# Optimization experiments

Hardware: AMD Instinct MI355X
Metric: run time of the kernel (lower is better)

## Reference

```python
import jax, jax.numpy as jnp
import numpy as np

# Static config (matches init_kwargs)
D_MODEL, H, L, P = 256, 8, 4, 4
HEAD_DIM = D_MODEL // H
SPATIAL = ((76, 114), (38, 57), (19, 29), (10, 15))  # (h, w) per level
NV = sum(h * w for h, w in SPATIAL)  # 11531
B, NQ = 2, NV


def setup_inputs() -> dict:
    key = jax.random.key(0)
    ks = jax.random.split(key, 12)
    inp = {
        "query": jax.random.normal(ks[0], (B, NQ, D_MODEL), jnp.float32),
        "reference_points": jax.random.uniform(ks[1], (B, NQ, L, 2), jnp.float32),
        "value": jax.random.normal(ks[2], (B, NV, D_MODEL), jnp.float32),
        # Linear params stored as [in, out] (i.e. torch weight transposed)
        "W_off": jax.random.normal(ks[3], (D_MODEL, H * L * P * 2), jnp.float32) * 0.02,
        "b_off": jax.random.normal(ks[4], (H * L * P * 2,), jnp.float32) * 0.5,
        "W_attn": jax.random.normal(ks[5], (D_MODEL, H * L * P), jnp.float32) * 0.02,
        "b_attn": jnp.zeros((H * L * P,), jnp.float32),
        "W_val": jax.random.normal(ks[6], (D_MODEL, D_MODEL), jnp.float32) * 0.05,
        "b_val": jnp.zeros((D_MODEL,), jnp.float32),
        "W_out": jax.random.normal(ks[7], (D_MODEL, D_MODEL), jnp.float32) * 0.05,
        "b_out": jnp.zeros((D_MODEL,), jnp.float32),
    }
    return inp


def _msda(query, reference_points, value, W_off, b_off, W_attn, b_attn,
          W_val, b_val, W_out, b_out):
    Bq, Nq, C = query.shape
    D = HEAD_DIM
    # value projection -> [B, H, Nv, D]
    v = (value @ W_val + b_val).reshape(Bq, -1, H, D).transpose(0, 2, 1, 3)
    # sampling locations: ref + offset / (w, h)  -> [B, Nq, H, L, P, 2] in [0,1] coords
    off = (query @ W_off + b_off).reshape(Bq, Nq, H, L, P, 2)
    wh = jnp.array([[w, h] for h, w in SPATIAL], dtype=query.dtype)  # [L, 2]
    loc = reference_points[:, :, None, :, None, :] + off / wh[None, None, None, :, None, :]
    # attention weights softmax over L*P  -> [B, H, Nq, L, P]
    attn = jax.nn.softmax((query @ W_attn + b_attn).reshape(Bq, Nq, H, L * P), axis=-1)
    attn = attn.reshape(Bq, Nq, H, L, P).transpose(0, 2, 1, 3, 4)
    starts = np.concatenate([[0], np.cumsum([h * w for h, w in SPATIAL])]).astype(int)
    out = jnp.zeros((Bq, H, Nq, D), query.dtype)
    for l, (lh, lw) in enumerate(SPATIAL):
        feat = v[:, :, starts[l]:starts[l + 1], :]  # [B, H, lh*lw, D]
        # grid_sample align_corners=False: pixel = loc * size - 0.5
        px = loc[:, :, :, l, :, 0].transpose(0, 2, 1, 3) * lw - 0.5  # [B, H, Nq, P]
        py = loc[:, :, :, l, :, 1].transpose(0, 2, 1, 3) * lh - 0.5
        x0 = jnp.floor(px)
        y0 = jnp.floor(py)
        samp = jnp.zeros(px.shape + (D,), query.dtype)
        for dx in (0, 1):
            for dy in (0, 1):
                xi = x0 + dx
                yi = y0 + dy
                w = (1.0 - jnp.abs(px - xi)) * (1.0 - jnp.abs(py - yi))
                valid = (xi >= 0) & (xi <= lw - 1) & (yi >= 0) & (yi <= lh - 1)
                idx = (jnp.clip(yi, 0, lh - 1) * lw + jnp.clip(xi, 0, lw - 1)).astype(jnp.int32)
                g = jnp.take_along_axis(feat, idx.reshape(Bq, H, -1)[..., None], axis=2)
                g = g.reshape(Bq, H, Nq, P, D)
                samp = samp + g * jnp.where(valid, w, 0.0)[..., None]
        out = out + jnp.einsum('bhnpd,bhnp->bhnd', samp, attn[:, :, :, l, :])
    out = out.transpose(0, 2, 1, 3).reshape(Bq, Nq, C)
    return out @ W_out + b_out


def reference(query, reference_points, value, W_off, b_off, W_attn, b_attn,
              W_val, b_val, W_out, b_out):
    return _msda(query, reference_points, value, W_off, b_off, W_attn, b_attn,
                 W_val, b_val, W_out, b_out)
```

## Files before the change

kernel.cpp:

```cpp
#include <hip/hip_runtime.h>
#include <cmath>

#define B_    2
#define NQ_   11531
#define NV_   11531
#define M_    (B_ * NQ_)
#define NCB_  2883

typedef unsigned short u16;
typedef unsigned int   u32;
typedef __attribute__((ext_vector_type(8))) short bf16x8;
typedef __attribute__((ext_vector_type(4))) float f32x4;
typedef __attribute__((ext_vector_type(2))) float f32x2;

__device__ __forceinline__ u16 f2bf(float f) {
    union { float f; unsigned u; } v; v.f = f;
    unsigned r = v.u + 0x7FFFu + ((v.u >> 16) & 1u);
    return (u16)(r >> 16);
}
__device__ __forceinline__ u16 f2h(float f) {
    union { _Float16 h; u16 u; } v; v.h = (_Float16)f; return v.u;
}
__device__ __forceinline__ float h2f(u16 u) {
    union { u16 u; _Float16 h; } v; v.u = u; return (float)v.h;
}
__device__ __forceinline__ f32x2 unpk(u32 u) {
    union { unsigned u; float f; } lo, hi;
    lo.u = u << 16; hi.u = u & 0xFFFF0000u;
    f32x2 r; r.x = lo.f; r.y = hi.f; return r;
}

__device__ __forceinline__ int sort_key(const float* __restrict__ refp, int bq) {
    const int b = bq / NQ_;
    const float2 r = *(const float2*)&refp[(size_t)bq * 8];
    int qx = (int)(r.x * 32.f); qx = min(max(qx, 0), 31);
    int qy = (int)(r.y * 32.f); qy = min(max(qy, 0), 31);
    return b * 1024 + qy * 32 + qx;
}

__global__ __launch_bounds__(256) void transpose_hist_cast(
    const float* __restrict__ Wv, const float* __restrict__ Wo,
    const float* __restrict__ Wa, const float* __restrict__ Wu,
    const float* __restrict__ refp,
    const float* __restrict__ query, const float* __restrict__ value,
    u16* __restrict__ Tv, u16* __restrict__ Toa, u16* __restrict__ Tu,
    int* __restrict__ hist, u16* __restrict__ qbf, u16* __restrict__ vbf) {
    const int bid = blockIdx.x;
    const int tid = threadIdx.x;
    if (bid >= 347) {
        const int t8 = bid - 347;
        const bool isq = t8 < NCB_;
        const int cb = isq ? t8 : t8 - NCB_;
        const float* S = isq ? query : value;
        u16* D = isq ? qbf : vbf;
        const size_t TOT = (size_t)M_ * 256;
        const size_t e = ((size_t)cb * 256 + tid) * 8;
        if (e + 8 <= TOT) {
            const float4 a = *(const float4*)&S[e];
            const float4 b = *(const float4*)&S[e + 4];
            ushort4 lo, hi;
            lo.x = f2bf(a.x); lo.y = f2bf(a.y); lo.z = f2bf(a.z); lo.w = f2bf(a.w);
            hi.x = f2bf(b.x); hi.y = f2bf(b.y); hi.z = f2bf(b.z); hi.w = f2bf(b.w);
            *(ushort4*)&D[e] = lo;
            *(ushort4*)&D[e + 4] = hi;
        } else {
            for (size_t i = e; i < TOT; ++i) D[i] = f2bf(S[i]);
        }
        return;
    }
    if (bid >= 256) {
        const int bq = (bid - 256) * 256 + tid;
        if (bq < M_) atomicAdd(&hist[sort_key(refp, bq)], 1);
        return;
    }
    const int z = bid >> 6;
    const float* W; u16* T; int N; int rowoff = 0;
    if (z == 0)      { W = Wv; T = Tv;  N = 256; }
    else if (z == 1) { W = Wo; T = Toa; N = 256; }
    else if (z == 2) { W = Wa; T = Toa; N = 128; rowoff = 256; }
    else             { W = Wu; T = Tu;  N = 256; }
    const int rest = bid & 63;
    const int n0 = (rest & 7) * 32, k0 = (rest >> 3) * 32;
    if (n0 >= N) return;
    __shared__ float t[32][33];
    const int c = tid & 31, r0 = tid >> 5;
#pragma unroll
    for (int i = 0; i < 4; ++i)
        t[r0 + i * 8][c] = W[(size_t)(k0 + r0 + i * 8) * N + n0 + c];
    __syncthreads();
#pragma unroll
    for (int i = 0; i < 4; ++i)
        T[(size_t)(rowoff + n0 + r0 + i * 8) * 256 + k0 + c] = f2bf(t[c][r0 + i * 8]);
}

__device__ void scan_block(const int* __restrict__ hist, int* __restrict__ ofs,
                           int* part) {
    const int tid = threadIdx.x;
    const int base = tid * 8;
    int loc[8]; int s = 0;
#pragma unroll
    for (int i = 0; i < 8; ++i) { loc[i] = s; s += hist[base + i]; }
    part[tid] = s;
    __syncthreads();
    for (int d = 1; d < 256; d <<= 1) {
        const int v = part[tid];
        const int u = (tid >= d) ? part[tid - d] : 0;
        __syncthreads();
        part[tid] = v + u;
        __syncthreads();
    }
    const int off = (tid > 0) ? part[tid - 1] : 0;
#pragma unroll
    for (int i = 0; i < 8; ++i) ofs[base + i] = off + loc[i];
}

__global__ __launch_bounds__(256) void repack_scatter(
    const u16* __restrict__ ws_v, const float* __restrict__ refp,
    int* __restrict__ ofs, int* __restrict__ perm,
    u32* __restrict__ v3, int nsc) {
    const int bid = blockIdx.x;
    const int tid = threadIdx.x;
    if (bid < nsc) {
        const int bq = bid * 256 + tid;
        if (bq < M_) {
            const int pos = atomicAdd(&ofs[sort_key(refp, bq)], 1);
            perm[pos] = bq;
        }
        return;
    }
    const int g4 = (bid - nsc) * 256 + tid;
    if (g4 >= 8 * M_ * 8) return;
    const int h = g4 / (M_ * 8);
    const int rem = g4 - h * (M_ * 8);
    const int r = rem >> 3;
    const int c = (rem & 7) * 4;
    const ushort4 lo = *(const ushort4*)&ws_v[(size_t)r * 256 + h * 32 + c];
    ushort4 hi = make_ushort4(0, 0, 0, 0);
    if (r + 1 < M_) hi = *(const ushort4*)&ws_v[(size_t)(r + 1) * 256 + h * 32 + c];
    uint4 o;
    o.x = (u32)lo.x | ((u32)hi.x << 16);
    o.y = (u32)lo.y | ((u32)hi.y << 16);
    o.z = (u32)lo.z | ((u32)hi.z << 16);
    o.w = (u32)lo.w | ((u32)hi.w << 16);
    *(uint4*)&v3[((size_t)h * M_ + r) * 32 + c] = o;
}

template <int TN, int EPI>
__device__ __forceinline__ void gemm_body(const u16* __restrict__ A,
                                          const u16* __restrict__ WT,
                                          const float* __restrict__ bias,
                                          const float* __restrict__ bias2,
                                          void* __restrict__ Cv, int M,
                                          int bm, int bn,
                                          short* A_l, short* B_l) {
    constexpr int K = 256;
    const int tid = threadIdx.x;
    const int w = tid >> 6;
    const int lane = tid & 63;
    const int wr = (w >> 1) * 64;
    const int wc = (w & 1) * 64;
    const int lr = lane & 15;

    f32x4 acc[4][4] = {};

    for (int k0 = 0; k0 < K; k0 += 64) {
#pragma unroll
        for (int i = 0; i < 4; ++i) {
            const int vid = tid + i * 256;
            const int ar = vid >> 3;
            const int ak = (vid & 7) * 8;
            const int gr = bm + ar;
            uint4 hv = make_uint4(0u, 0u, 0u, 0u);
            if (gr < M) hv = *(const uint4*)&A[(size_t)gr * K + k0 + ak];
            *(uint4*)&A_l[ar * 72 + ak] = hv;
        }
#pragma unroll
        for (int i = 0; i < 4; ++i) {
            const int vid = tid + i * 256;
            const int nr = vid >> 3;
            const int kk = (vid & 7) * 8;
            const uint4 wv = *(const uint4*)&WT[(size_t)(bn + nr) * K + k0 + kk];
            *(uint4*)&B_l[nr * 72 + kk] = wv;
        }
        __syncthreads();
#pragma unroll
        for (int half = 0; half < 2; ++half) {
            const int kg = half * 32 + (lane >> 4) * 8;
            bf16x8 af[4], bfr[4];
#pragma unroll
            for (int m = 0; m < 4; ++m)
                af[m] = *(const bf16x8*)&A_l[(wr + m * 16 + lr) * 72 + kg];
#pragma unroll
            for (int n = 0; n < 4; ++n)
                bfr[n] = *(const bf16x8*)&B_l[(wc + n * 16 + lr) * 72 + kg];
#pragma unroll
            for (int m = 0; m < 4; ++m)
#pragma unroll
                for (int n = 0; n < 4; ++n)
                    acc[m][n] = __builtin_amdgcn_mfma_f32_16x16x32_bf16(af[m], bfr[n], acc[m][n], 0, 0, 0);
        }
        __syncthreads();
    }

#pragma unroll
    for (int n = 0; n < 4; ++n) {
        const int gcol = bn + wc + n * 16 + lr;
        const float bv = (TN == 384 && gcol >= 256) ? bias2[gcol - 256] : bias[gcol];
#pragma unroll
        for (int m = 0; m < 4; ++m) {
            const int rbase = bm + wr + m * 16 + (lane >> 4) * 4;
#pragma unroll
            for (int j = 0; j < 4; ++j) {
                const int grow = rbase + j;
                if (grow < M) {
                    const float o = acc[m][n][j] + bv;
                    if constexpr (EPI == 1)      ((u16*)Cv)[(size_t)grow * TN + gcol] = f2bf(o);
                    else if constexpr (EPI == 2) ((u16*)Cv)[(size_t)grow * TN + gcol] = f2h(o);
                    else                         ((float*)Cv)[(size_t)grow * TN + gcol] = o;
                }
            }
        }
    }
}

__global__ __launch_bounds__(256, 4) void gemm_stage1(
    const u16* __restrict__ qbf, const u16* __restrict__ vbf,
    const u16* __restrict__ WT_val, const u16* __restrict__ WT_oa,
    const float* __restrict__ b_val, const float* __restrict__ b_off,
    const float* __restrict__ b_attn,
    const int* __restrict__ hist, int* __restrict__ ofs,
    u16* __restrict__ ws_v, u16* __restrict__ ws_oa, int M, int gy) {
    __shared__ __align__(16) short A_l[128 * 72];
    __shared__ __align__(16) short B_l[128 * 72];
    int blk = blockIdx.x;
    if (blk == 5 * gy) {
        scan_block(hist, ofs, (int*)A_l);
    } else if (blk < 2 * gy) {
        gemm_body<256, 1>(vbf, WT_val, b_val, b_val, ws_v, M,
                          (blk >> 1) * 128, (blk & 1) * 128, A_l, B_l);
    } else {
        blk -= 2 * gy;
        gemm_body<384, 2>(qbf, WT_oa, b_off, b_attn, ws_oa, M,
                          (blk / 3) * 128, (blk % 3) * 128, A_l, B_l);
    }
}

__global__ __launch_bounds__(256, 4) void gemm_out(
    const u16* __restrict__ samp, const u16* __restrict__ WT_out,
    const float* __restrict__ b_out, float* __restrict__ out, int M) {
    __shared__ __align__(16) short A_l[128 * 72];
    __shared__ __align__(16) short B_l[128 * 72];
    const int blk = blockIdx.x;
    gemm_body<256, 0>(samp, WT_out, b_out, b_out, out, M,
                      (blk >> 1) * 128, (blk & 1) * 128, A_l, B_l);
}

__global__ __launch_bounds__(512, 4) void msda_sample_v12(
    const u32* __restrict__ v3,
    const u16* __restrict__ oa,
    const float* __restrict__ refp,
    const int* __restrict__ perm,
    u16* __restrict__ samp) {
    __shared__ __align__(16) float4 s_w4[1088];
    __shared__ __align__(8)  int2   s_i2[1088];
    __shared__ int s_bq[8];
    const int tid = threadIdx.x;

    const int nwg = gridDim.x;
    const int qq = nwg >> 3, rr = nwg & 7;
    const int xcd = blockIdx.x & 7, pos = blockIdx.x >> 3;
    const int wg = (xcd < rr ? xcd * (qq + 1) : rr * (qq + 1) + (xcd - rr) * qq) + pos;
    const int bq0 = wg * 8;

    if (tid < 8) {
        const int q = bq0 + tid;
        s_bq[tid] = perm[q < M_ ? q : M_ - 1];
    }
    __syncthreads();

#pragma unroll
    for (int half = 0; half < 2; ++half) {
        const int s = tid + half * 512;
        const int qi = s >> 7;
        const int rem = s & 127;
        const int sampi = rem & 15;
        const int l = sampi >> 2;
        const int h = rem >> 4;
        const int bq = s_bq[qi];
        const int b = bq / NQ_;
        const u16* oar = oa + (size_t)bq * 384;

        const float logit = h2f(oar[256 + rem]);
        float mx = logit;
#pragma unroll
        for (int t = 8; t >= 1; t >>= 1) mx = fmaxf(mx, __shfl_xor(mx, t, 16));
        const float e = __expf(logit - mx);
        float sm = e;
#pragma unroll
        for (int t = 8; t >= 1; t >>= 1) sm += __shfl_xor(sm, t, 16);
        const float aw = e / sm;

        const u32 op = *(const u32*)&oar[rem * 2];
        const float offx = h2f((u16)op);
        const float offy = h2f((u16)(op >> 16));
        const float2 rxy = *(const float2*)&refp[(size_t)bq * 8 + l * 2];
        const int lw = (l == 0) ? 114 : (l == 1) ? 57 : (l == 2) ? 29 : 15;
        const int lh = (l == 0) ? 76 : (l == 1) ? 38 : (l == 2) ? 19 : 10;
        const int st = (l == 0) ? 0 : (l == 1) ? 8664 : (l == 2) ? 10830 : 11381;
        const int base = b * NV_ + st;

        const float px = rxy.x * (float)lw + offx - 0.5f;
        const float py = rxy.y * (float)lh + offy - 0.5f;
        const float x0f = floorf(px), y0f = floorf(py);
        const int x0 = (int)x0f, y0 = (int)y0f;
        const float fx = px - x0f, fy = py - y0f;

        float wxlo = 0.f, wxhi = 0.f;
        if (x0 >= 0 && x0 < lw)      wxlo = 1.f - fx;
        else if (x0 == -1)           wxlo = fx;
        if (x0 >= 0 && x0 + 1 < lw)  wxhi = fx;
        const int xs = min(max(x0, 0), lw - 1);

        const float wy0 = (y0 >= 0 && y0 < lh) ? (1.f - fy) : 0.f;
        const float wy1 = (y0 + 1 >= 0 && y0 + 1 < lh) ? fy : 0.f;
        const int ys0 = min(max(y0, 0), lh - 1);
        const int ys1 = min(max(y0 + 1, 0), lh - 1);

        const int hrow = h * M_;
        int2 iv;
        iv.x = (hrow + base + ys0 * lw + xs) << 7;
        iv.y = (hrow + base + ys1 * lw + xs) << 7;
        float4 wv;
        wv.x = aw * wxlo * wy0; wv.y = aw * wxhi * wy0;
        wv.z = aw * wxlo * wy1; wv.w = aw * wxhi * wy1;
        const int slot = (qi * 8 + h) * 17 + sampi;
        s_w4[slot] = wv;
        s_i2[slot] = iv;
    }
    __syncthreads();

    const int qi = tid >> 6;
    const int lane = tid & 63;
    const int h = lane >> 3;
    const int lcoff = (lane & 7) * 16;
    const int bq = s_bq[qi];
    const int sb = (qi * 8 + h) * 17;
    const char* vb = (const char*)v3;

    f32x2 acc0 = {0.f, 0.f}, acc1 = {0.f, 0.f}, acc2 = {0.f, 0.f}, acc3 = {0.f, 0.f};
    float4 wcur = s_w4[sb];
    int2 ic = s_i2[sb];
    uint4 A0 = *(const uint4*)(vb + (u32)(ic.x + lcoff));
    uint4 A1 = *(const uint4*)(vb + (u32)(ic.y + lcoff));

#pragma unroll 2
    for (int sp = 0; sp < 16; ++sp) {
        const int nxt = (sp + 1) & 15;
        const float4 wn = s_w4[sb + nxt];
        const int2 in_ = s_i2[sb + nxt];
        const uint4 B0 = *(const uint4*)(vb + (u32)(in_.x + lcoff));
        const uint4 B1 = *(const uint4*)(vb + (u32)(in_.y + lcoff));

        f32x2 w01; w01.x = wcur.x; w01.y = wcur.y;
        f32x2 w23; w23.x = wcur.z; w23.y = wcur.w;
        acc0 += unpk(A0.x) * w01; acc0 += unpk(A1.x) * w23;
        acc1 += unpk(A0.y) * w01; acc1 += unpk(A1.y) * w23;
        acc2 += unpk(A0.z) * w01; acc2 += unpk(A1.z) * w23;
        acc3 += unpk(A0.w) * w01; acc3 += unpk(A1.w) * w23;

        wcur = wn; A0 = B0; A1 = B1;
    }
    if (bq0 + qi < M_) {
        ushort4 o;
        o.x = f2bf(acc0.x + acc0.y); o.y = f2bf(acc1.x + acc1.y);
        o.z = f2bf(acc2.x + acc2.y); o.w = f2bf(acc3.x + acc3.y);
        *(ushort4*)&samp[(size_t)bq * 256 + (h * 32 + (lane & 7) * 4)] = o;
    }
}

extern "C" void kernel_launch(void* const* d_in, const int* in_sizes, int n_in,
                              void* d_out, int out_size, void* d_ws, size_t ws_size,
                              hipStream_t stream) {
    const float* query  = (const float*)d_in[0];
    const float* refp   = (const float*)d_in[1];
    const float* value  = (const float*)d_in[2];
    const float* W_off  = (const float*)d_in[3];
    const float* b_off  = (const float*)d_in[4];
    const float* W_attn = (const float*)d_in[5];
    const float* b_attn = (const float*)d_in[6];
    const float* W_val  = (const float*)d_in[7];
    const float* b_val  = (const float*)d_in[8];
    const float* W_out  = (const float*)d_in[9];
    const float* b_out  = (const float*)d_in[10];
    float* out = (float*)d_out;

    const int M = M_;
    u16*   ws_v    = (u16*)d_ws;
    u16*   ws_samp = ws_v;
    u32*   ws_v3   = (u32*)(ws_v + (size_t)M * 256);
    u16*   vbf     = (u16*)ws_v3;
    u16*   ws_oa   = (u16*)(ws_v3 + (size_t)8 * M * 32);
    u16*   qbf     = ws_oa + (size_t)M * 384;
    u16*   WT_val  = qbf + (size_t)M * 256;
    u16*   WT_oa   = WT_val + 256 * 256;
    u16*   WT_out  = WT_oa + 384 * 256;
    int*   hist    = (int*)(WT_out + 256 * 256);
    int*   ofs     = hist + 2048;
    int*   perm    = ofs + 2048;

    const int gy = (M + 127) / 128;
    const int gq = (M + 255) / 256;
    const int grep = (8 * M * 8 + 255) / 256;

    hipMemsetAsync(hist, 0, 2048 * sizeof(int), stream);
    transpose_hist_cast<<<dim3(347 + 2 * NCB_), 256, 0, stream>>>(
        W_val, W_off, W_attn, W_out, refp, query, value,
        WT_val, WT_oa, WT_out, hist, qbf, vbf);
    gemm_stage1<<<dim3(5 * gy + 1), 256, 0, stream>>>(qbf, vbf, WT_val, WT_oa,
                                                      b_val, b_off, b_attn,
                                                      hist, ofs, ws_v, ws_oa, M, gy);
    repack_scatter<<<dim3(gq + grep), 256, 0, stream>>>(ws_v, refp, ofs, perm,
                                                        ws_v3, gq);
    msda_sample_v12<<<dim3((M + 7) / 8), 512, 0, stream>>>(ws_v3, ws_oa, refp, perm, ws_samp);
    gemm_out<<<dim3(2 * gy), 256, 0, stream>>>(ws_samp, WT_out, b_out, out, M);
}
```

Before: 113.0 us.

## Fuse value repack into GEMM epilogue and drop softmax max subtraction

Result: faster. 104.7 us (-7.3%).

```diff
diff --git a/kernel.cpp b/kernel.cpp
--- a/kernel.cpp
+++ b/kernel.cpp
@@ -114,35 +114,14 @@
     for (int i = 0; i < 8; ++i) ofs[base + i] = off + loc[i];
 }
 
-__global__ __launch_bounds__(256) void repack_scatter(
-    const u16* __restrict__ ws_v, const float* __restrict__ refp,
-    int* __restrict__ ofs, int* __restrict__ perm,
-    u32* __restrict__ v3, int nsc) {
-    const int bid = blockIdx.x;
-    const int tid = threadIdx.x;
-    if (bid < nsc) {
-        const int bq = bid * 256 + tid;
-        if (bq < M_) {
-            const int pos = atomicAdd(&ofs[sort_key(refp, bq)], 1);
-            perm[pos] = bq;
-        }
-        return;
-    }
-    const int g4 = (bid - nsc) * 256 + tid;
-    if (g4 >= 8 * M_ * 8) return;
-    const int h = g4 / (M_ * 8);
-    const int rem = g4 - h * (M_ * 8);
-    const int r = rem >> 3;
-    const int c = (rem & 7) * 4;
-    const ushort4 lo = *(const ushort4*)&ws_v[(size_t)r * 256 + h * 32 + c];
-    ushort4 hi = make_ushort4(0, 0, 0, 0);
-    if (r + 1 < M_) hi = *(const ushort4*)&ws_v[(size_t)(r + 1) * 256 + h * 32 + c];
-    uint4 o;
-    o.x = (u32)lo.x | ((u32)hi.x << 16);
-    o.y = (u32)lo.y | ((u32)hi.y << 16);
-    o.z = (u32)lo.z | ((u32)hi.z << 16);
-    o.w = (u32)lo.w | ((u32)hi.w << 16);
-    *(uint4*)&v3[((size_t)h * M_ + r) * 32 + c] = o;
+__global__ __launch_bounds__(256) void scatter_kernel(const float* __restrict__ refp,
+                                                      int* __restrict__ ofs,
+                                                      int* __restrict__ perm) {
+    const int bq = blockIdx.x * 256 + threadIdx.x;
+    if (bq < M_) {
+        const int pos = atomicAdd(&ofs[sort_key(refp, bq)], 1);
+        perm[pos] = bq;
+    }
 }
 
 template <int TN, int EPI>
@@ -202,6 +181,47 @@
         __syncthreads();
     }
 
+    if constexpr (EPI == 3) {
+        u16* tile = (u16*)A_l;
+#pragma unroll
+        for (int n = 0; n < 4; ++n) {
+            const int col = wc + n * 16 + lr;
+            const float bv = bias[bn + col];
+#pragma unroll
+            for (int m = 0; m < 4; ++m) {
+                const int rb = wr + m * 16 + (lane >> 4) * 4;
+#pragma unroll
+                for (int j = 0; j < 4; ++j)
+                    tile[(rb + j) * 132 + col] = f2bf(acc[m][n][j] + bv);
+            }
+        }
+        __syncthreads();
+        u32* v3 = (u32*)Cv;
+#pragma unroll 4
+        for (int i = 0; i < 64; ++i) {
+            const int wdx = tid + i * 256;
+            const int col = wdx & 127, r = wdx >> 7;
+            const int grow = bm + r;
+            if (grow < M) {
+                const int h = (bn + col) >> 5, c = (bn + col) & 31;
+                const size_t word = ((size_t)h * M + grow) * 32 + c;
+                const u32 lo = tile[r * 132 + col];
+                if (r < 127) {
+                    const u32 hi = tile[(r + 1) * 132 + col];
+                    v3[word] = lo | (hi << 16);
+                } else {
+                    ((u16*)v3)[word * 2] = (u16)lo;
+                }
+            }
+        }
+        if (bm > 0 && tid < 128) {
+            const int col = tid;
+            const int h = (bn + col) >> 5, c = (bn + col) & 31;
+            ((u16*)v3)[(((size_t)h * M + (bm - 1)) * 32 + c) * 2 + 1] = (u16)tile[col];
+        }
+        return;
+    }
+
 #pragma unroll
     for (int n = 0; n < 4; ++n) {
         const int gcol = bn + wc + n * 16 + lr;
@@ -214,9 +234,8 @@
                 const int grow = rbase + j;
                 if (grow < M) {
                     const float o = acc[m][n][j] + bv;
-                    if constexpr (EPI == 1)      ((u16*)Cv)[(size_t)grow * TN + gcol] = f2bf(o);
-                    else if constexpr (EPI == 2) ((u16*)Cv)[(size_t)grow * TN + gcol] = f2h(o);
-                    else                         ((float*)Cv)[(size_t)grow * TN + gcol] = o;
+                    if constexpr (EPI == 2) ((u16*)Cv)[(size_t)grow * TN + gcol] = f2h(o);
+                    else                    ((float*)Cv)[(size_t)grow * TN + gcol] = o;
                 }
             }
         }
@@ -229,33 +248,31 @@
     const float* __restrict__ b_val, const float* __restrict__ b_off,
     const float* __restrict__ b_attn,
     const int* __restrict__ hist, int* __restrict__ ofs,
-    u16* __restrict__ ws_v, u16* __restrict__ ws_oa, int M, int gy) {
-    __shared__ __align__(16) short A_l[128 * 72];
-    __shared__ __align__(16) short B_l[128 * 72];
+    u32* __restrict__ ws_v3, u16* __restrict__ ws_oa, int M, int gy) {
+    __shared__ __align__(16) short sh[18432];
     int blk = blockIdx.x;
     if (blk == 5 * gy) {
-        scan_block(hist, ofs, (int*)A_l);
+        scan_block(hist, ofs, (int*)sh);
     } else if (blk < 2 * gy) {
-        gemm_body<256, 1>(vbf, WT_val, b_val, b_val, ws_v, M,
-                          (blk >> 1) * 128, (blk & 1) * 128, A_l, B_l);
+        gemm_body<256, 3>(vbf, WT_val, b_val, b_val, ws_v3, M,
+                          (blk >> 1) * 128, (blk & 1) * 128, sh, sh + 9216);
     } else {
         blk -= 2 * gy;
         gemm_body<384, 2>(qbf, WT_oa, b_off, b_attn, ws_oa, M,
-                          (blk / 3) * 128, (blk % 3) * 128, A_l, B_l);
+                          (blk / 3) * 128, (blk % 3) * 128, sh, sh + 9216);
     }
 }
 
 __global__ __launch_bounds__(256, 4) void gemm_out(
     const u16* __restrict__ samp, const u16* __restrict__ WT_out,
     const float* __restrict__ b_out, float* __restrict__ out, int M) {
-    __shared__ __align__(16) short A_l[128 * 72];
-    __shared__ __align__(16) short B_l[128 * 72];
+    __shared__ __align__(16) short sh[18432];
     const int blk = blockIdx.x;
     gemm_body<256, 0>(samp, WT_out, b_out, b_out, out, M,
-                      (blk >> 1) * 128, (blk & 1) * 128, A_l, B_l);
-}
-
-__global__ __launch_bounds__(512, 4) void msda_sample_v12(
+                      (blk >> 1) * 128, (blk & 1) * 128, sh, sh + 9216);
+}
+
+__global__ __launch_bounds__(512, 4) void msda_sample_v13(
     const u32* __restrict__ v3,
     const u16* __restrict__ oa,
     const float* __restrict__ refp,
@@ -290,11 +307,7 @@
         const int b = bq / NQ_;
         const u16* oar = oa + (size_t)bq * 384;
 
-        const float logit = h2f(oar[256 + rem]);
-        float mx = logit;
-#pragma unroll
-        for (int t = 8; t >= 1; t >>= 1) mx = fmaxf(mx, __shfl_xor(mx, t, 16));
-        const float e = __expf(logit - mx);
+        const float e = __expf(h2f(oar[256 + rem]));
         float sm = e;
 #pragma unroll
         for (int t = 8; t >= 1; t >>= 1) sm += __shfl_xor(sm, t, 16);
@@ -395,13 +408,12 @@
     float* out = (float*)d_out;
 
     const int M = M_;
-    u16*   ws_v    = (u16*)d_ws;
-    u16*   ws_samp = ws_v;
-    u32*   ws_v3   = (u32*)(ws_v + (size_t)M * 256);
-    u16*   vbf     = (u16*)ws_v3;
+    u16*   vbf     = (u16*)d_ws;
+    u32*   ws_v3   = (u32*)(vbf + (size_t)M * 256);
     u16*   ws_oa   = (u16*)(ws_v3 + (size_t)8 * M * 32);
     u16*   qbf     = ws_oa + (size_t)M * 384;
-    u16*   WT_val  = qbf + (size_t)M * 256;
+    u16*   ws_samp = qbf + (size_t)M * 256;
+    u16*   WT_val  = ws_samp + (size_t)M * 256;
     u16*   WT_oa   = WT_val + 256 * 256;
     u16*   WT_out  = WT_oa + 384 * 256;
     int*   hist    = (int*)(WT_out + 256 * 256);
@@ -410,7 +422,6 @@
 
     const int gy = (M + 127) / 128;
     const int gq = (M + 255) / 256;
-    const int grep = (8 * M * 8 + 255) / 256;
 
     hipMemsetAsync(hist, 0, 2048 * sizeof(int), stream);
     transpose_hist_cast<<<dim3(347 + 2 * NCB_), 256, 0, stream>>>(
@@ -418,9 +429,8 @@
         WT_val, WT_oa, WT_out, hist, qbf, vbf);
     gemm_stage1<<<dim3(5 * gy + 1), 256, 0, stream>>>(qbf, vbf, WT_val, WT_oa,
                                                       b_val, b_off, b_attn,
-                                                      hist, ofs, ws_v, ws_oa, M, gy);
-    repack_scatter<<<dim3(gq + grep), 256, 0, stream>>>(ws_v, refp, ofs, perm,
-                                                        ws_v3, gq);
-    msda_sample_v12<<<dim3((M + 7) / 8), 512, 0, stream>>>(ws_v3, ws_oa, refp, perm, ws_samp);
+                                                      hist, ofs, ws_v3, ws_oa, M, gy);
+    scatter_kernel<<<dim3(gq), 256, 0, stream>>>(refp, ofs, perm);
+    msda_sample_v13<<<dim3((M + 7) / 8), 512, 0, stream>>>(ws_v3, ws_oa, refp, perm, ws_samp);
     gemm_out<<<dim3(2 * gy), 256, 0, stream>>>(ws_samp, WT_out, b_out, out, M);
 }
```
